# Kernel tuning notes

Hardware: AMD Instinct MI355X
Metric: run time of the kernel (lower is better)

Reference implementation:

```python
import jax, jax.numpy as jnp
import numpy as np

NEG_INF = -1e9


def setup_inputs() -> dict:
    key0 = jax.random.key(0)
    ks = jax.random.split(key0, 7)
    B, Tq, Tv, D, U = 8, 512, 512, 512, 128
    query = jax.random.normal(ks[0], (B, Tq, D), dtype=jnp.float32)
    key = jax.random.normal(ks[1], (B, Tv, D), dtype=jnp.float32)
    value = jax.random.normal(ks[2], (B, Tv, D), dtype=jnp.float32)
    mask = jax.random.randint(ks[3], (B, Tv), 0, 2).astype(bool)
    mask = mask.at[:, 0].set(True)  # ensure no fully-masked row
    Wa = jax.random.normal(ks[4], (D, U), dtype=jnp.float32) * (1.0 / np.sqrt(D))
    Ua = jax.random.normal(ks[5], (D, U), dtype=jnp.float32) * (1.0 / np.sqrt(D))
    scale = jax.random.normal(ks[6], (U,), dtype=jnp.float32) * 0.1
    return {"query": query, "key": key, "value": value, "mask": mask,
            "Wa": Wa, "Ua": Ua, "scale": scale}


def reference(query, key, value, mask, Wa, Ua, scale):
    # Dense projections (no bias)
    q = query @ Wa          # [B, Tq, U]
    k = key @ Ua            # [B, Tv, U]
    # Additive (Bahdanau) scores with learned per-unit scale:
    # scores[b,i,j] = sum_u scale[u] * tanh(q[b,i,u] + k[b,j,u])
    t = jnp.tanh(q[:, :, None, :] + k[:, None, :, :])   # [B, Tq, Tv, U]
    scores = jnp.einsum('bijU,U->bij', t, scale)         # [B, Tq, Tv]
    # Mask padded keys/values then softmax over Tv
    scores = jnp.where(mask[:, None, :], scores, NEG_INF)
    weights = jax.nn.softmax(scores, axis=-1)            # [B, Tq, Tv]
    # Weighted sum of values (query_mask is all-True in source -> no-op)
    context = jnp.einsum('bij,bjd->bid', weights, value) # [B, Tq, D]
    return context
```

## Files before the change

kernel.cpp:

```cpp
#include <hip/hip_runtime.h>

constexpr int Bb = 8;
constexpr int Tq = 512;
constexpr int Tv = 512;
constexpr int Dd = 512;
constexpr int Uu = 128;
constexpr float C2LOG2E = 2.88539008177792681f;
constexpr float LOG2E   = 1.44269504088896341f;

__global__ __launch_bounds__(256) void proj_kernel(
    const float* __restrict__ query,
    const float* __restrict__ key,
    const float* __restrict__ Wa,
    const float* __restrict__ Ua,
    const int* __restrict__ mask,
    float* __restrict__ qf2, float* __restrict__ kT)
{
    const int R    = blockIdx.x * 16;
    const bool isQ = R < Bb * Tq;
    const float* __restrict__ src = isQ ? query : key;
    const float* __restrict__ W   = isQ ? Wa : Ua;
    const int Rloc = isQ ? R : R - Bb * Tq;

    __shared__ float x[16 * Dd];
    __shared__ int posLoc[16];
    const int t = threadIdx.x;

    {
        const float4* __restrict__ s4 =
            reinterpret_cast<const float4*>(src + (size_t)Rloc * Dd);
        float4* x4 = reinterpret_cast<float4*>(x);
#pragma unroll
        for (int m = 0; m < 8; ++m) x4[t + 256 * m] = s4[t + 256 * m];
    }
    if (!isQ && t < 64) {
        const int b  = Rloc >> 9;
        const int j0 = Rloc & 511;
        int base = 0;
#pragma unroll
        for (int c = 0; c < 8; ++c) {
            const int j = c * 64 + t;
            const int v = (mask[b * 512 + j] != 0);
            const unsigned long long bits = __ballot(v);
            const int pos = base + (int)__popcll(bits & ((1ull << t) - 1ull));
            if (j >= j0 && j < j0 + 16) posLoc[j - j0] = v ? pos : -1;
            base += (int)__popcll(bits);
        }
    }
    __syncthreads();

    const int ub = t & 63;
    const int rh = t >> 6;
    float acc[4][2] = {{0,0},{0,0},{0,0},{0,0}};

#pragma unroll 2
    for (int d4 = 0; d4 < Dd / 4; ++d4) {
        const int d = d4 * 4;
        const float w0x = W[(d + 0) * Uu + ub],      w1x = W[(d + 0) * Uu + ub + 64];
        const float w0y = W[(d + 1) * Uu + ub],      w1y = W[(d + 1) * Uu + ub + 64];
        const float w0z = W[(d + 2) * Uu + ub],      w1z = W[(d + 2) * Uu + ub + 64];
        const float w0w = W[(d + 3) * Uu + ub],      w1w = W[(d + 3) * Uu + ub + 64];
#pragma unroll
        for (int k = 0; k < 4; ++k) {
            const float4 xv = *reinterpret_cast<const float4*>(x + (rh * 4 + k) * Dd + d);
            acc[k][0] = fmaf(xv.x, w0x, acc[k][0]);
            acc[k][0] = fmaf(xv.y, w0y, acc[k][0]);
            acc[k][0] = fmaf(xv.z, w0z, acc[k][0]);
            acc[k][0] = fmaf(xv.w, w0w, acc[k][0]);
            acc[k][1] = fmaf(xv.x, w1x, acc[k][1]);
            acc[k][1] = fmaf(xv.y, w1y, acc[k][1]);
            acc[k][1] = fmaf(xv.z, w1z, acc[k][1]);
            acc[k][1] = fmaf(xv.w, w1w, acc[k][1]);
        }
    }

    if (isQ) {
#pragma unroll
        for (int k = 0; k < 4; ++k) {
            const size_t row = (size_t)(Rloc + rh * 4 + k);
            qf2[row * Uu + ub]      = C2LOG2E * acc[k][0];
            qf2[row * Uu + ub + 64] = C2LOG2E * acc[k][1];
        }
    } else {
        float* __restrict__ kb = kT + (size_t)(Rloc >> 9) * Uu * Tv;
#pragma unroll
        for (int k = 0; k < 4; ++k) {
            const int p = posLoc[rh * 4 + k];
            if (p >= 0) {
                kb[(size_t)ub        * Tv + p] = C2LOG2E * acc[k][0];
                kb[(size_t)(ub + 64) * Tv + p] = C2LOG2E * acc[k][1];
            }
        }
    }
}

__global__ __launch_bounds__(512) void attn_kernel(
    const float* __restrict__ qf2, const float* __restrict__ kT,
    const float* __restrict__ value,
    const int* __restrict__ mask,
    const float* __restrict__ scale,
    float* __restrict__ out)
{
    const int r0 = blockIdx.x * 8;
    const int b  = r0 >> 9;
    const int t  = threadIdx.x;

    __shared__ float q2[8 * Uu];
    __shared__ float s2[Uu];
    __shared__ int   jl[Tv];
    __shared__ float w[8 * Tv];
    __shared__ float pbuf[8 * Dd];
    __shared__ float inv8[8];
    __shared__ int   cntS;

    jl[t] = 0;
    if (t < 256)
        reinterpret_cast<float4*>(q2)[t] =
            reinterpret_cast<const float4*>(qf2 + (size_t)r0 * Uu)[t];
    else if (t < 384) s2[t - 256] = scale[t - 256];
    __syncthreads();
    if (t < 64) {
        int base = 0;
#pragma unroll
        for (int c = 0; c < 8; ++c) {
            const int j = c * 64 + t;
            const int v = (mask[b * 512 + j] != 0);
            const unsigned long long bits = __ballot(v);
            const int pos = base + (int)__popcll(bits & ((1ull << t) - 1ull));
            if (v) jl[pos] = j;
            base += (int)__popcll(bits);
        }
        if (t == 0) cntS = base;
    }
    __syncthreads();

    const int cnt   = cntS;
    const int cntp4 = (cnt + 3) & ~3;

    const int s   = t & 255;
    const int rh  = t >> 8;
    const float* __restrict__ qh = q2 + rh * 4 * Uu;
    float* __restrict__ wh = w + rh * 4 * Tv;
    const int niter = (cntp4 + 255) >> 8;
    for (int it = 0; it < niter; ++it) {
        const int jc = s + it * 256;
        if (jc < cnt) {
            const float* __restrict__ kb = kT + (size_t)b * Uu * Tv + jc;
            float acc[4] = {0, 0, 0, 0};
#pragma unroll 2
            for (int u4 = 0; u4 < Uu / 4; ++u4) {
                const float kx = kb[(size_t)(u4 * 4 + 0) * Tv];
                const float ky = kb[(size_t)(u4 * 4 + 1) * Tv];
                const float kz = kb[(size_t)(u4 * 4 + 2) * Tv];
                const float kw = kb[(size_t)(u4 * 4 + 3) * Tv];
                const float4 sv = reinterpret_cast<const float4*>(s2)[u4];
#pragma unroll
                for (int i = 0; i < 4; ++i) {
                    const float4 qv = *reinterpret_cast<const float4*>(qh + i * Uu + u4 * 4);
                    float e0 = __builtin_amdgcn_exp2f(qv.x + kx);
                    float e1 = __builtin_amdgcn_exp2f(qv.y + ky);
                    float e2 = __builtin_amdgcn_exp2f(qv.z + kz);
                    float e3 = __builtin_amdgcn_exp2f(qv.w + kw);
                    acc[i] = fmaf(sv.x, __builtin_amdgcn_rcpf(e0 + 1.f), acc[i]);
                    acc[i] = fmaf(sv.y, __builtin_amdgcn_rcpf(e1 + 1.f), acc[i]);
                    acc[i] = fmaf(sv.z, __builtin_amdgcn_rcpf(e2 + 1.f), acc[i]);
                    acc[i] = fmaf(sv.w, __builtin_amdgcn_rcpf(e3 + 1.f), acc[i]);
                }
            }
#pragma unroll
            for (int i = 0; i < 4; ++i) wh[i * Tv + jc] = -2.f * acc[i];
        } else if (jc < cntp4) {
#pragma unroll
            for (int i = 0; i < 4; ++i) wh[i * Tv + jc] = 0.f;
        }
    }
    __syncthreads();

    {
        const int wv = t >> 6, ln = t & 63;
        float* __restrict__ row = w + wv * Tv;
        float vals[8];
        float m = -3e38f;
#pragma unroll
        for (int c = 0; c < 8; ++c) {
            const int e = ln + 64 * c;
            vals[c] = (e < cnt) ? row[e] : -3e38f;
            m = fmaxf(m, vals[c]);
        }
#pragma unroll
        for (int off = 32; off; off >>= 1) m = fmaxf(m, __shfl_xor(m, off, 64));
        float sum = 0.f;
#pragma unroll
        for (int c = 0; c < 8; ++c) {
            const int e = ln + 64 * c;
            if (e < cnt) {
                float ex = __builtin_amdgcn_exp2f((vals[c] - m) * LOG2E);
                row[e] = ex;
                sum += ex;
            }
        }
#pragma unroll
        for (int off = 32; off; off >>= 1) sum += __shfl_xor(sum, off, 64);
        if (ln == 0) inv8[wv] = 1.0f / sum;
    }
    __syncthreads();

    const int mid  = ((cntp4 >> 1) + 3) & ~3;
    const int g  = t >> 8;
    const int c  = t & 255;
    const int d0 = c * 2;
    const int jbeg = g ? mid : 0;
    const int jend = g ? cntp4 : mid;
    const float* __restrict__ vb = value + (size_t)b * Tv * Dd + d0;
    float ax[8], ay[8];
#pragma unroll
    for (int i = 0; i < 8; ++i) { ax[i] = 0.f; ay[i] = 0.f; }

    for (int jj = jbeg; jj < jend; jj += 4) {
        const int4 rows = *reinterpret_cast<const int4*>(jl + jj);
        const float2 v0 = *reinterpret_cast<const float2*>(vb + (size_t)rows.x * Dd);
        const float2 v1 = *reinterpret_cast<const float2*>(vb + (size_t)rows.y * Dd);
        const float2 v2 = *reinterpret_cast<const float2*>(vb + (size_t)rows.z * Dd);
        const float2 v3 = *reinterpret_cast<const float2*>(vb + (size_t)rows.w * Dd);
#pragma unroll
        for (int i = 0; i < 8; ++i) {
            const float4 wq = *reinterpret_cast<const float4*>(w + i * Tv + jj);
            ax[i] = fmaf(wq.x, v0.x, ax[i]); ay[i] = fmaf(wq.x, v0.y, ay[i]);
            ax[i] = fmaf(wq.y, v1.x, ax[i]); ay[i] = fmaf(wq.y, v1.y, ay[i]);
            ax[i] = fmaf(wq.z, v2.x, ax[i]); ay[i] = fmaf(wq.z, v2.y, ay[i]);
            ax[i] = fmaf(wq.w, v3.x, ax[i]); ay[i] = fmaf(wq.w, v3.y, ay[i]);
        }
    }

    if (g == 1) {
#pragma unroll
        for (int i = 0; i < 8; ++i) {
            float2 p; p.x = ax[i]; p.y = ay[i];
            *reinterpret_cast<float2*>(pbuf + i * Dd + d0) = p;
        }
    }
    __syncthreads();
    if (g == 0) {
#pragma unroll
        for (int i = 0; i < 8; ++i) {
            const float inv = inv8[i];
            const float2 p1 = *reinterpret_cast<const float2*>(pbuf + i * Dd + d0);
            float2 o;
            o.x = (ax[i] + p1.x) * inv;
            o.y = (ay[i] + p1.y) * inv;
            *reinterpret_cast<float2*>(out + (size_t)(r0 + i) * Dd + d0) = o;
        }
    }
}

extern "C" void kernel_launch(void* const* d_in, const int* in_sizes, int n_in,
                              void* d_out, int out_size, void* d_ws, size_t ws_size,
                              hipStream_t stream)
{
    const float* query = (const float*)d_in[0];
    const float* key   = (const float*)d_in[1];
    const float* value = (const float*)d_in[2];
    const int*   mask  = (const int*)d_in[3];
    const float* Wa    = (const float*)d_in[4];
    const float* Ua    = (const float*)d_in[5];
    const float* scale = (const float*)d_in[6];
    float* out = (float*)d_out;

    float* qf2 = (float*)d_ws;
    float* kT  = qf2 + Bb * Tq * Uu;

    proj_kernel<<<(2 * Bb * Tq) / 16, 256, 0, stream>>>(query, key, Wa, Ua, mask, qf2, kT);
    attn_kernel<<<(Bb * Tq) / 8, 512, 0, stream>>>(qf2, kT, value, mask, scale, out);
}
```

Before: 171.0 us.

## Shrink attention blocks to 4 query rows with 256 threads

The attention kernel now has each block handle 4 query rows with 256 threads, where it previously handled 8 rows with 512 threads. This doubles the grid to 1024 blocks and drops the split-Tv partial-sum buffer and its extra barrier in the context stage. Shared memory per block shrinks, which allows more resident blocks per CU. In exchange, K columns and value rows are reloaded twice as often across blocks, since each load now serves only 4 query rows.

```diff
diff --git a/kernel.cpp b/kernel.cpp
--- a/kernel.cpp
+++ b/kernel.cpp
@@ -94,30 +94,29 @@
     }
 }
 
-__global__ __launch_bounds__(512) void attn_kernel(
+__global__ __launch_bounds__(256, 4) void attn_kernel(
     const float* __restrict__ qf2, const float* __restrict__ kT,
     const float* __restrict__ value,
     const int* __restrict__ mask,
     const float* __restrict__ scale,
     float* __restrict__ out)
 {
-    const int r0 = blockIdx.x * 8;
+    const int r0 = blockIdx.x * 4;
     const int b  = r0 >> 9;
     const int t  = threadIdx.x;
 
-    __shared__ float q2[8 * Uu];
+    __shared__ float q2[4 * Uu];
     __shared__ float s2[Uu];
     __shared__ int   jl[Tv];
-    __shared__ float w[8 * Tv];
-    __shared__ float pbuf[8 * Dd];
-    __shared__ float inv8[8];
+    __shared__ float w[4 * Tv];
+    __shared__ float inv4[4];
     __shared__ int   cntS;
 
-    jl[t] = 0;
-    if (t < 256)
+    jl[t] = 0; jl[t + 256] = 0;
+    if (t < 128)
         reinterpret_cast<float4*>(q2)[t] =
             reinterpret_cast<const float4*>(qf2 + (size_t)r0 * Uu)[t];
-    else if (t < 384) s2[t - 256] = scale[t - 256];
+    else s2[t - 128] = scale[t - 128];
     __syncthreads();
     if (t < 64) {
         int base = 0;
@@ -137,13 +136,9 @@
     const int cnt   = cntS;
     const int cntp4 = (cnt + 3) & ~3;
 
-    const int s   = t & 255;
-    const int rh  = t >> 8;
-    const float* __restrict__ qh = q2 + rh * 4 * Uu;
-    float* __restrict__ wh = w + rh * 4 * Tv;
     const int niter = (cntp4 + 255) >> 8;
     for (int it = 0; it < niter; ++it) {
-        const int jc = s + it * 256;
+        const int jc = t + it * 256;
         if (jc < cnt) {
             const float* __restrict__ kb = kT + (size_t)b * Uu * Tv + jc;
             float acc[4] = {0, 0, 0, 0};
@@ -156,7 +151,7 @@
                 const float4 sv = reinterpret_cast<const float4*>(s2)[u4];
 #pragma unroll
                 for (int i = 0; i < 4; ++i) {
-                    const float4 qv = *reinterpret_cast<const float4*>(qh + i * Uu + u4 * 4);
+                    const float4 qv = *reinterpret_cast<const float4*>(q2 + i * Uu + u4 * 4);
                     float e0 = __builtin_amdgcn_exp2f(qv.x + kx);
                     float e1 = __builtin_amdgcn_exp2f(qv.y + ky);
                     float e2 = __builtin_amdgcn_exp2f(qv.z + kz);
@@ -168,10 +163,10 @@
                 }
             }
 #pragma unroll
-            for (int i = 0; i < 4; ++i) wh[i * Tv + jc] = -2.f * acc[i];
+            for (int i = 0; i < 4; ++i) w[i * Tv + jc] = -2.f * acc[i];
         } else if (jc < cntp4) {
 #pragma unroll
-            for (int i = 0; i < 4; ++i) wh[i * Tv + jc] = 0.f;
+            for (int i = 0; i < 4; ++i) w[i * Tv + jc] = 0.f;
         }
     }
     __syncthreads();
@@ -201,29 +196,24 @@
         }
 #pragma unroll
         for (int off = 32; off; off >>= 1) sum += __shfl_xor(sum, off, 64);
-        if (ln == 0) inv8[wv] = 1.0f / sum;
-    }
-    __syncthreads();
-
-    const int mid  = ((cntp4 >> 1) + 3) & ~3;
-    const int g  = t >> 8;
-    const int c  = t & 255;
-    const int d0 = c * 2;
-    const int jbeg = g ? mid : 0;
-    const int jend = g ? cntp4 : mid;
+        if (ln == 0) inv4[wv] = 1.0f / sum;
+    }
+    __syncthreads();
+
+    const int d0 = t * 2;
     const float* __restrict__ vb = value + (size_t)b * Tv * Dd + d0;
-    float ax[8], ay[8];
-#pragma unroll
-    for (int i = 0; i < 8; ++i) { ax[i] = 0.f; ay[i] = 0.f; }
-
-    for (int jj = jbeg; jj < jend; jj += 4) {
+    float ax[4], ay[4];
+#pragma unroll
+    for (int i = 0; i < 4; ++i) { ax[i] = 0.f; ay[i] = 0.f; }
+
+    for (int jj = 0; jj < cntp4; jj += 4) {
         const int4 rows = *reinterpret_cast<const int4*>(jl + jj);
         const float2 v0 = *reinterpret_cast<const float2*>(vb + (size_t)rows.x * Dd);
         const float2 v1 = *reinterpret_cast<const float2*>(vb + (size_t)rows.y * Dd);
         const float2 v2 = *reinterpret_cast<const float2*>(vb + (size_t)rows.z * Dd);
         const float2 v3 = *reinterpret_cast<const float2*>(vb + (size_t)rows.w * Dd);
 #pragma unroll
-        for (int i = 0; i < 8; ++i) {
+        for (int i = 0; i < 4; ++i) {
             const float4 wq = *reinterpret_cast<const float4*>(w + i * Tv + jj);
             ax[i] = fmaf(wq.x, v0.x, ax[i]); ay[i] = fmaf(wq.x, v0.y, ay[i]);
             ax[i] = fmaf(wq.y, v1.x, ax[i]); ay[i] = fmaf(wq.y, v1.y, ay[i]);
@@ -232,24 +222,13 @@
         }
     }
 
-    if (g == 1) {
-#pragma unroll
-        for (int i = 0; i < 8; ++i) {
-            float2 p; p.x = ax[i]; p.y = ay[i];
-            *reinterpret_cast<float2*>(pbuf + i * Dd + d0) = p;
-        }
-    }
-    __syncthreads();
-    if (g == 0) {
-#pragma unroll
-        for (int i = 0; i < 8; ++i) {
-            const float inv = inv8[i];
-            const float2 p1 = *reinterpret_cast<const float2*>(pbuf + i * Dd + d0);
-            float2 o;
-            o.x = (ax[i] + p1.x) * inv;
-            o.y = (ay[i] + p1.y) * inv;
-            *reinterpret_cast<float2*>(out + (size_t)(r0 + i) * Dd + d0) = o;
-        }
+#pragma unroll
+    for (int i = 0; i < 4; ++i) {
+        const float inv = inv4[i];
+        float2 o;
+        o.x = ax[i] * inv;
+        o.y = ay[i] * inv;
+        *reinterpret_cast<float2*>(out + (size_t)(r0 + i) * Dd + d0) = o;
     }
 }
 
@@ -270,5 +249,5 @@
     float* kT  = qf2 + Bb * Tq * Uu;
 
     proj_kernel<<<(2 * Bb * Tq) / 16, 256, 0, stream>>>(query, key, Wa, Ua, mask, qf2, kT);
-    attn_kernel<<<(Bb * Tq) / 8, 512, 0, stream>>>(qf2, kT, value, mask, scale, out);
+    attn_kernel<<<(Bb * Tq) / 4, 256, 0, stream>>>(qf2, kT, value, mask, scale, out);
 }
```

Result: no change. 168.2 us (-1.6%).

## Interleave projected keys by four units and give each thread one key for eight queries

Applied to the files above, without the earlier changes.

The key projection is now stored in a layout that groups four units per key, so the score loop can fetch them with a single float4 load instead of four strided scalar loads. The score phase also changes its work split: each of the 512 threads handles one compacted key for all 8 query rows, rather than 256 threads each covering 4 rows and looping over keys. Each thread reads its key data once and reuses it across 8 rows, but it now holds more accumulators and no longer loops when the count is small. Threads whose key index is at or past the count write zeros, covering the whole row.

```diff
diff --git a/kernel.cpp b/kernel.cpp
--- a/kernel.cpp
+++ b/kernel.cpp
@@ -83,12 +83,13 @@
         }
     } else {
         float* __restrict__ kb = kT + (size_t)(Rloc >> 9) * Uu * Tv;
+        const int u4a = ub >> 2, ca = ub & 3;
 #pragma unroll
         for (int k = 0; k < 4; ++k) {
             const int p = posLoc[rh * 4 + k];
             if (p >= 0) {
-                kb[(size_t)ub        * Tv + p] = C2LOG2E * acc[k][0];
-                kb[(size_t)(ub + 64) * Tv + p] = C2LOG2E * acc[k][1];
+                kb[(size_t)(u4a        * Tv + p) * 4 + ca] = C2LOG2E * acc[k][0];
+                kb[(size_t)((u4a + 16) * Tv + p) * 4 + ca] = C2LOG2E * acc[k][1];
             }
         }
     }
@@ -137,42 +138,33 @@
     const int cnt   = cntS;
     const int cntp4 = (cnt + 3) & ~3;
 
-    const int s   = t & 255;
-    const int rh  = t >> 8;
-    const float* __restrict__ qh = q2 + rh * 4 * Uu;
-    float* __restrict__ wh = w + rh * 4 * Tv;
-    const int niter = (cntp4 + 255) >> 8;
-    for (int it = 0; it < niter; ++it) {
-        const int jc = s + it * 256;
-        if (jc < cnt) {
-            const float* __restrict__ kb = kT + (size_t)b * Uu * Tv + jc;
-            float acc[4] = {0, 0, 0, 0};
+    const int jc = t;
+    if (jc < cnt) {
+        const float4* __restrict__ kb4 =
+            reinterpret_cast<const float4*>(kT) + (size_t)b * 32 * Tv + jc;
+        float acc[8] = {0,0,0,0,0,0,0,0};
 #pragma unroll 2
-            for (int u4 = 0; u4 < Uu / 4; ++u4) {
-                const float kx = kb[(size_t)(u4 * 4 + 0) * Tv];
-                const float ky = kb[(size_t)(u4 * 4 + 1) * Tv];
-                const float kz = kb[(size_t)(u4 * 4 + 2) * Tv];
-                const float kw = kb[(size_t)(u4 * 4 + 3) * Tv];
-                const float4 sv = reinterpret_cast<const float4*>(s2)[u4];
-#pragma unroll
-                for (int i = 0; i < 4; ++i) {
-                    const float4 qv = *reinterpret_cast<const float4*>(qh + i * Uu + u4 * 4);
-                    float e0 = __builtin_amdgcn_exp2f(qv.x + kx);
-                    float e1 = __builtin_amdgcn_exp2f(qv.y + ky);
-                    float e2 = __builtin_amdgcn_exp2f(qv.z + kz);
-                    float e3 = __builtin_amdgcn_exp2f(qv.w + kw);
-                    acc[i] = fmaf(sv.x, __builtin_amdgcn_rcpf(e0 + 1.f), acc[i]);
-                    acc[i] = fmaf(sv.y, __builtin_amdgcn_rcpf(e1 + 1.f), acc[i]);
-                    acc[i] = fmaf(sv.z, __builtin_amdgcn_rcpf(e2 + 1.f), acc[i]);
-                    acc[i] = fmaf(sv.w, __builtin_amdgcn_rcpf(e3 + 1.f), acc[i]);
-                }
+        for (int u4 = 0; u4 < Uu / 4; ++u4) {
+            const float4 kv = kb4[(size_t)u4 * Tv];
+            const float4 sv = reinterpret_cast<const float4*>(s2)[u4];
+#pragma unroll
+            for (int i = 0; i < 8; ++i) {
+                const float4 qv = *reinterpret_cast<const float4*>(q2 + i * Uu + u4 * 4);
+                float e0 = __builtin_amdgcn_exp2f(qv.x + kv.x);
+                float e1 = __builtin_amdgcn_exp2f(qv.y + kv.y);
+                float e2 = __builtin_amdgcn_exp2f(qv.z + kv.z);
+                float e3 = __builtin_amdgcn_exp2f(qv.w + kv.w);
+                acc[i] = fmaf(sv.x, __builtin_amdgcn_rcpf(e0 + 1.f), acc[i]);
+                acc[i] = fmaf(sv.y, __builtin_amdgcn_rcpf(e1 + 1.f), acc[i]);
+                acc[i] = fmaf(sv.z, __builtin_amdgcn_rcpf(e2 + 1.f), acc[i]);
+                acc[i] = fmaf(sv.w, __builtin_amdgcn_rcpf(e3 + 1.f), acc[i]);
             }
-#pragma unroll
-            for (int i = 0; i < 4; ++i) wh[i * Tv + jc] = -2.f * acc[i];
-        } else if (jc < cntp4) {
-#pragma unroll
-            for (int i = 0; i < 4; ++i) wh[i * Tv + jc] = 0.f;
-        }
+        }
+#pragma unroll
+        for (int i = 0; i < 8; ++i) w[i * Tv + jc] = -2.f * acc[i];
+    } else {
+#pragma unroll
+        for (int i = 0; i < 8; ++i) w[i * Tv + jc] = 0.f;
     }
     __syncthreads();
 
@@ -205,7 +197,7 @@
     }
     __syncthreads();
 
-    const int mid  = ((cntp4 >> 1) + 3) & ~3;
+    const int mid = ((cntp4 >> 1) + 3) & ~3;
     const int g  = t >> 8;
     const int c  = t & 255;
     const int d0 = c * 2;
```

After: 165.0 us. -3.5%, faster.
